# Kernel optimization log

Hardware: AMD Instinct MI355X
Metric: run time of the kernel (lower is better)

Reference implementation:

```python
import jax, jax.numpy as jnp
import numpy as np
import math

T, N, F, A, NH = 2048, 64, 64, 64, 8
QG, QH, DG, DH = 256, 256, 256, 256
HORIZON = 16


def setup_inputs() -> dict:
    key = jax.random.key(0)
    ks = jax.random.split(key, 12)
    s = 0.05  # xavier-ish scale
    return {
        "x_fix": jax.random.normal(ks[0], (T, F), jnp.float32),
        "x_att": jax.random.normal(ks[1], (T, N, A), jnp.float32),
        "train_horizon": HORIZON,
        # query GRUCell: input = fix + 2*A*NH
        "q_gru_w_ih": jax.random.normal(ks[2], (3 * QG, F + 2 * A * NH), jnp.float32) * s,
        "q_gru_w_hh": jax.random.normal(ks[3], (3 * QG, QG), jnp.float32) * s,
        "q_gru_b_ih": jnp.zeros((3 * QG,), jnp.float32),
        "q_gru_b_hh": jnp.zeros((3 * QG,), jnp.float32),
        # q_hidden: input = QG + F + A*NH
        "q_hid_w": jax.random.normal(ks[4], (QH, QG + F + A * NH), jnp.float32) * s,
        "q_hid_b": jnp.zeros((QH,), jnp.float32),
        "weight_q": jax.random.normal(ks[5], (QH, A * NH), jnp.float32) * s,
        # decoder GRU: input = F + A*NH
        "dec_gru_w_ih": jax.random.normal(ks[6], (3 * DG, F + A * NH), jnp.float32) * s,
        "dec_gru_w_hh": jax.random.normal(ks[7], (3 * DG, DG), jnp.float32) * s,
        "dec_gru_b_ih": jnp.zeros((3 * DG,), jnp.float32),
        "dec_gru_b_hh": jnp.zeros((3 * DG,), jnp.float32),
        # dec_hidden: input = DG + F + A*NH + A
        "dec_hid_w": jax.random.normal(ks[8], (DH, DG + F + A * NH + A), jnp.float32) * s,
        "dec_hid_b": jnp.zeros((DH,), jnp.float32),
        "dec_out_w": jax.random.normal(ks[9], (A, DH), jnp.float32) * s,
        "dec_out_b": jnp.zeros((A,), jnp.float32),
    }


def _gru_cell(x, h, w_ih, w_hh, b_ih, b_hh):
    """PyTorch GRUCell math (gate order r,z,n)."""
    gi = w_ih @ x + b_ih
    gh = w_hh @ h + b_hh
    ir, iz, in_ = jnp.split(gi, 3)
    hr, hz, hn = jnp.split(gh, 3)
    r = jax.nn.sigmoid(ir + hr)
    z = jax.nn.sigmoid(iz + hz)
    n = jnp.tanh(in_ + r * hn)
    return (1.0 - z) * n + z * h


def reference(x_fix, x_att, train_horizon,
              q_gru_w_ih, q_gru_w_hh, q_gru_b_ih, q_gru_b_hh,
              q_hid_w, q_hid_b, weight_q,
              dec_gru_w_ih, dec_gru_w_hh, dec_gru_b_ih, dec_gru_b_hh,
              dec_hid_w, dec_hid_b, dec_out_w, dec_out_b):
    t, n_obj, a = x_att.shape
    nh_a = weight_q.shape[1]
    nh = nh_a // a
    scale = 1.0 / math.sqrt(a)

    # ---- recurrent query generation (sequential over time) ----
    def step(carry, inp):
        h, query = carry
        fix_t, att_t = inp                                   # [F], [N, A]
        attw = jax.nn.softmax((query.reshape(nh, a) @ att_t.T) * scale, axis=1)  # [NH, N]
        att_v = (attw @ att_t).reshape(-1)                   # [NH*A]
        h2 = _gru_cell(jnp.concatenate([fix_t, att_v, query]), h,
                       q_gru_w_ih, q_gru_w_hh, q_gru_b_ih, q_gru_b_hh)
        hid = jax.nn.relu(q_hid_w @ jnp.concatenate([h2, fix_t, att_v]) + q_hid_b)
        query2 = hid @ weight_q
        return (h2, query2), (attw, att_v)

    h0 = jnp.zeros((q_gru_w_hh.shape[1],), x_fix.dtype)
    q0 = jnp.ones((nh_a,), x_fix.dtype)
    (q_gru_n, query_n), (attw, att_a) = jax.lax.scan(step, (h0, q0), (x_fix, x_att))

    # ---- decoder (training path; dropout_p=0, noise_std=0 -> identity) ----
    hz = train_horizon
    # replicate-pad attw back hz steps in time, drop last hz: dec_attw[t] = attw[max(t-hz,0)]
    dec_attw = jnp.concatenate(
        [jnp.broadcast_to(attw[:1], (hz,) + attw.shape[1:]), attw[:-hz]], axis=0)  # [T, NH, N]
    dec_att_a = jnp.einsum('thn,tnd->thd', dec_attw, x_att).reshape(t, -1)          # [T, NH*A]
    dec_x = jnp.concatenate([x_fix, dec_att_a], axis=-1)                            # [T, F+NH*A]

    def dec_step(hd, xt):
        hd2 = _gru_cell(xt, hd, dec_gru_w_ih, dec_gru_w_hh, dec_gru_b_ih, dec_gru_b_hh)
        return hd2, hd2

    dg0 = jnp.zeros((dec_gru_w_hh.shape[1],), x_fix.dtype)
    dec_gru_n, dec_gru_a = jax.lax.scan(dec_step, dg0, dec_x)                       # [T, DG]

    feat = jnp.concatenate([dec_gru_a, dec_x], axis=-1)                             # [T, DG+F+NH*A]
    feat_b = jnp.broadcast_to(feat[:, None, :], (t, n_obj, feat.shape[-1]))
    inp = jnp.concatenate([feat_b, x_att], axis=-1)                                 # [T, N, DG+F+NH*A+A]
    hid = jax.nn.relu(inp @ dec_hid_w.T + dec_hid_b)
    pred = jax.nn.relu(hid @ dec_out_w.T + dec_out_b)                               # [T, N, A]

    return pred, attw, q_gru_n, dec_gru_n, query_n
```

## Files before the change

kernel.cpp:

```cpp
#include <hip/hip_runtime.h>
#include <math.h>

#define TT 2048
#define HZ 16
#define NBLK 32
#define NTH 512

#define OUT_ATTW   (2048*64*64)
#define OUT_QGRU   (OUT_ATTW + 2048*8*64)
#define OUT_DECGRU (OUT_QGRU + 256)
#define OUT_QN     (OUT_DECGRU + 256)

#define WSO_MB1    0
#define WSO_QACC   8192
#define WSO_QCNT   14336
#define WSO_ZEND   14464
#define WSO_GIFIX  14464
#define WSO_HIDFIX (WSO_GIFIX + 2048*768*4)
#define WSO_W2T    (WSO_HIDFIX + 2048*256*4)
#define WSO_DAVA   (WSO_W2T + 256*64*4)
#define WSO_DECH   (WSO_DAVA + 2048*512*4)
#define WSO_FEAT   (WSO_DECH + 2048*256*4)
#define WSO_SBUF   (WSO_FEAT + 2048*832*4)

__device__ __forceinline__ float warp_sum(float v) {
#pragma unroll
  for (int o = 32; o > 0; o >>= 1) v += __shfl_down(v, o, 64);
  return v;
}
__device__ __forceinline__ float warp_max(float v) {
#pragma unroll
  for (int o = 32; o > 0; o >>= 1) v = fmaxf(v, __shfl_down(v, o, 64));
  return v;
}
__device__ __forceinline__ float sigf(float x) { return 1.f / (1.f + __expf(-x)); }
__device__ __forceinline__ float dot4(float4 a, float4 b) {
  return a.x*b.x + a.y*b.y + a.z*b.z + a.w*b.w;
}
__device__ __forceinline__ unsigned long long aload64(const unsigned long long* p) {
  return __hip_atomic_load(p, __ATOMIC_RELAXED, __HIP_MEMORY_SCOPE_AGENT);
}
__device__ __forceinline__ void astore64(unsigned long long* p, unsigned long long v) {
  __hip_atomic_store(p, v, __ATOMIC_RELAXED, __HIP_MEMORY_SCOPE_AGENT);
}
__device__ __forceinline__ unsigned long long mbpack(float f, unsigned tag) {
  return ((unsigned long long)tag << 32) | (unsigned long long)__float_as_uint(f);
}
__device__ __forceinline__ float mbpoll(const unsigned long long* p, unsigned tag) {
  unsigned long long v = aload64(p);
  while ((unsigned)(v >> 32) != tag) {
    __builtin_amdgcn_s_sleep(1);
    v = aload64(p);
  }
  return __uint_as_float((unsigned)v);
}

__global__ void transpose_k(const float* __restrict__ w2,
                            float* __restrict__ w2T) {
  int e = blockIdx.x * 256 + threadIdx.x;
  int r = e >> 6, a = e & 63;
  w2T[e] = w2[a * 256 + r];
}

__global__ void __launch_bounds__(256) gemm64(
    const float* __restrict__ X, int ldx,
    const float* __restrict__ W, int ldw, int woff,
    const float* __restrict__ bias,
    float* __restrict__ C, int crows, int K) {
  __shared__ float Xs[64 * 65];
  __shared__ float Ws[64 * 65];
  int t0 = blockIdx.x * 64, r0 = blockIdx.y * 64;
  int tid = threadIdx.x;
  int u = tid & 15, v = tid >> 4;
  float acc[4][4];
#pragma unroll
  for (int i = 0; i < 4; i++)
#pragma unroll
    for (int j = 0; j < 4; j++) acc[i][j] = 0.f;

  for (int kc = 0; kc < K; kc += 64) {
    for (int idx = tid; idx < 4096; idx += 256) {
      int row = idx >> 6, col = idx & 63;
      Xs[row * 65 + col] = X[(size_t)(t0 + row) * ldx + kc + col];
      Ws[row * 65 + col] = W[(size_t)(r0 + row) * ldw + woff + kc + col];
    }
    __syncthreads();
#pragma unroll 8
    for (int k = 0; k < 64; k++) {
      float xs[4], ws[4];
#pragma unroll
      for (int i = 0; i < 4; i++) xs[i] = Xs[(v + 16 * i) * 65 + k];
#pragma unroll
      for (int j = 0; j < 4; j++) ws[j] = Ws[(u + 16 * j) * 65 + k];
#pragma unroll
      for (int i = 0; i < 4; i++)
#pragma unroll
        for (int j = 0; j < 4; j++) acc[i][j] += xs[i] * ws[j];
    }
    __syncthreads();
  }
#pragma unroll
  for (int i = 0; i < 4; i++)
#pragma unroll
    for (int j = 0; j < 4; j++) {
      int t = t0 + v + 16 * i, r = r0 + u + 16 * j;
      C[(size_t)t * crows + r] = acc[i][j] + bias[r];
    }
}

__global__ void __launch_bounds__(512) seq_kernel(
    const float* __restrict__ x_fix,
    const float* __restrict__ x_att,
    const float* __restrict__ w_ih,
    const float* __restrict__ w_hh,
    const float* __restrict__ b_hh,
    const float* __restrict__ q_hid_w,
    const float* __restrict__ wq,
    const float* __restrict__ dwih,
    const float* __restrict__ dwhh,
    const float* __restrict__ dbih,
    const float* __restrict__ dbhh,
    const float* __restrict__ gi_fix,
    const float* __restrict__ hid_fix,
    unsigned long long* __restrict__ mb1,
    float* __restrict__ qacc,
    unsigned* __restrict__ qcnt,
    float* __restrict__ dava,
    float* __restrict__ dec_hist,
    float* __restrict__ out) {
  __shared__ float att_s[64 * 65];
  __shared__ float ring_s[16][512];
  __shared__ __align__(16) float avq_s[1024];
  __shared__ float qk_s[512];
  __shared__ __align__(16) float xcat_s[576];
  __shared__ __align__(16) float hid8_s[8];
  __shared__ __align__(16) float h_s[256];
  __shared__ __align__(16) float dech_s[256];
  __shared__ float g_s[4][8];
  __shared__ float dg_s[4][8];

  const int tid = threadIdx.x;
  const int bid = blockIdx.x;
  const int lane = tid & 63, wv = tid >> 6;

  int rowsQ[3];
#pragma unroll
  for (int k = 0; k < 3; k++) {
    int m = wv * 3 + k;
    rowsQ[k] = ((m >> 3) * 256) + bid * 8 + (m & 7);
  }

  float4 wGi[3][4];
  float4 wGh[3];
  float bhh_r[3], dbi_r[3], dbh_r[3];
#pragma unroll
  for (int k = 0; k < 3; k++) {
    const float4* Wi = (const float4*)(w_ih + (size_t)rowsQ[k] * 1088 + 64);
#pragma unroll
    for (int c0 = 0; c0 < 4; c0++) wGi[k][c0] = Wi[lane + 64 * c0];
    wGh[k] = ((const float4*)(w_hh + (size_t)rowsQ[k] * 256))[lane];
    bhh_r[k] = b_hh[rowsQ[k]];
    dbi_r[k] = dbih[rowsQ[k]];
    dbh_r[k] = dbhh[rowsQ[k]];
  }
  float4 wBq[3];
  {
    const float4* W = (const float4*)(q_hid_w + (size_t)(bid * 8 + wv) * 832);
    wBq[0] = W[lane];
    wBq[1] = W[80 + lane];
    wBq[2] = W[144 + lane];
  }
  float wqr[8];
#pragma unroll
  for (int r = 0; r < 8; r++) wqr[r] = wq[(size_t)(bid * 8 + r) * 512 + tid];

  auto dec_gates = [&]() {
    float accg[3], acch[3];
#pragma unroll
    for (int k = 0; k < 3; k++) { accg[k] = 0.f; acch[k] = 0.f; }
    const float4* x4 = (const float4*)xcat_s;
#pragma unroll
    for (int c0 = 0; c0 < 3; c0++) {
      int c = lane + 64 * c0;
      if (c < 144) {
        float4 v = x4[c];
#pragma unroll
        for (int k = 0; k < 3; k++) {
          const float4* W = (const float4*)(dwih + (size_t)rowsQ[k] * 576);
          accg[k] += dot4(W[c], v);
        }
      }
    }
    {
      float4 vh = ((const float4*)dech_s)[lane];
#pragma unroll
      for (int k = 0; k < 3; k++) {
        const float4* Wh = (const float4*)(dwhh + (size_t)rowsQ[k] * 256);
        acch[k] += dot4(Wh[lane], vh);
      }
    }
#pragma unroll
    for (int k = 0; k < 3; k++) {
      int m = wv * 3 + k;
      int gate = m >> 3, idx = m & 7;
      if (gate < 2) {
        float s = warp_sum(accg[k] + acch[k]);
        if (lane == 0) dg_s[gate][idx] = s + dbi_r[k] + dbh_r[k];
      } else {
        float sg = warp_sum(accg[k]);
        float sh = warp_sum(acch[k]);
        if (lane == 0) { dg_s[2][idx] = sg + dbi_r[k]; dg_s[3][idx] = sh + dbh_r[k]; }
      }
    }
  };

  for (int i = tid; i < 1024; i += NTH) avq_s[i] = (i >= 512) ? 1.f : 0.f;
  if (tid < 256) { h_s[tid] = 0.f; dech_s[tid] = 0.f; }
  {
    const float4* g4 = (const float4*)x_att;
    float4 a = g4[tid * 2], b = g4[tid * 2 + 1];
    int row = tid >> 3, c0 = (tid & 7) * 8;
    float* d = &att_s[row * 65 + c0];
    d[0]=a.x; d[1]=a.y; d[2]=a.z; d[3]=a.w; d[4]=b.x; d[5]=b.y; d[6]=b.z; d[7]=b.w;
  }
  if (tid < 64) xcat_s[tid] = x_fix[tid];
  __syncthreads();

  for (int t = 0; t <= TT; ++t) {
    if (t > 0) {
      {
        float f = mbpoll(mb1 + (size_t)((t - 1) & 1) * 512 + tid, (unsigned)t);
        int b = tid >> 4, j = tid & 15;
        if (j < 8) h_s[b * 8 + j] = f;
        else dech_s[b * 8 + j - 8] = f;
        if (t >= 2 && tid < 16)
          __hip_atomic_store(&qacc[(size_t)((t - 1) % 3) * 512 + bid * 16 + tid],
                             0.f, __ATOMIC_RELAXED, __HIP_MEMORY_SCOPE_AGENT);
      }
      __syncthreads();
      {
        float hfx = hid_fix[(size_t)(t - 1) * 256 + bid * 8 + wv];
        const float4* h4 = (const float4*)h_s;
        const float4* a4 = (const float4*)avq_s;
        float acc = dot4(wBq[0], h4[lane]) + dot4(wBq[1], a4[lane]) +
                    dot4(wBq[2], a4[64 + lane]);
        float s = warp_sum(acc);
        if (lane == 0) hid8_s[wv] = fmaxf(s + hfx, 0.f);
      }
      __syncthreads();
      {
        float hv[8];
#pragma unroll
        for (int r = 0; r < 8; r++) hv[r] = hid8_s[r];
        float partial = 0.f;
#pragma unroll
        for (int r = 0; r < 8; r++) partial += hv[r] * wqr[r];
        __hip_atomic_fetch_add(&qacc[(size_t)(t % 3) * 512 + tid], partial,
                               __ATOMIC_RELAXED, __HIP_MEMORY_SCOPE_AGENT);
        asm volatile("s_waitcnt vmcnt(0)" ::: "memory");
      }
      __syncthreads();
      if (tid == 0)
        __hip_atomic_fetch_add(qcnt, 1u, __ATOMIC_RELAXED,
                               __HIP_MEMORY_SCOPE_AGENT);
      if (t < TT) {
        {
          const float* rg = ring_s[(t >= 16) ? (t & 15) : 0];
          float dv = 0.f;
#pragma unroll 8
          for (int n = 0; n < 64; n++) dv += rg[wv * 64 + n] * att_s[n * 65 + lane];
          xcat_s[64 + wv * 64 + lane] = dv;
        }
        __syncthreads();
        dec_gates();
        __syncthreads();
        if (tid < 8) {
          float r = sigf(dg_s[0][tid]), z = sigf(dg_s[1][tid]);
          float nn = tanhf(dg_s[2][tid] + r * dg_s[3][tid]);
          float d2 = (1.f - z) * nn + z * dech_s[bid * 8 + tid];
          astore64(&mb1[(size_t)(t & 1) * 512 + bid * 16 + 8 + tid],
                   mbpack(d2, (unsigned)(t + 1)));
          dec_hist[(size_t)t * 256 + bid * 8 + tid] = d2;
        } else if (tid >= 16 && tid < 32) {
          int k2 = tid - 16;
          dava[(size_t)t * 512 + bid * 16 + k2] = xcat_s[64 + bid * 16 + k2];
        }
      }
      if (tid == 0) {
        unsigned target = 32u * (unsigned)t;
        while (__hip_atomic_load(qcnt, __ATOMIC_RELAXED,
                                 __HIP_MEMORY_SCOPE_AGENT) < target)
          __builtin_amdgcn_s_sleep(1);
      }
      __syncthreads();
      {
        float qv = __hip_atomic_load(&qacc[(size_t)(t % 3) * 512 + tid],
                                     __ATOMIC_RELAXED, __HIP_MEMORY_SCOPE_AGENT);
        avq_s[512 + tid] = qv;
        if (t == TT) {
          if (bid == 0) {
            if (tid < 256) {
              out[OUT_QGRU + tid] = h_s[tid];
              out[OUT_DECGRU + tid] = dech_s[tid];
            }
            out[OUT_QN + tid] = qv;
          }
          break;
        }
      }
      __syncthreads();
    }

    float4 pfa, pfb;
    {
      int tn = (t + 1 < TT) ? t + 1 : t;
      const float4* g4 = (const float4*)(x_att + (size_t)tn * 4096);
      pfa = g4[tid * 2];
      pfb = g4[tid * 2 + 1];
    }
    float gfx[3];
#pragma unroll
    for (int k = 0; k < 3; k++) gfx[k] = gi_fix[(size_t)t * 768 + rowsQ[k]];
    {
      float acc = 0.f;
#pragma unroll 16
      for (int a = 0; a < 64; a++)
        acc += avq_s[512 + wv * 64 + a] * att_s[lane * 65 + a];
      acc *= 0.125f;
      float m = __shfl(warp_max(acc), 0, 64);
      float e = __expf(acc - m);
      float s = __shfl(warp_sum(e), 0, 64);
      qk_s[wv * 64 + lane] = e / s;
    }
    {
      float av = 0.f;
#pragma unroll 8
      for (int n = 0; n < 64; n++)
        av += qk_s[wv * 64 + n] * att_s[n * 65 + lane];
      avq_s[wv * 64 + lane] = av;
    }
    if (t == 0) {
      float dv = 0.f;
#pragma unroll 8
      for (int n = 0; n < 64; n++)
        dv += qk_s[wv * 64 + n] * att_s[n * 65 + lane];
      xcat_s[64 + wv * 64 + lane] = dv;
    }
    __syncthreads();
    {
      float accg[3], acch[3];
#pragma unroll
      for (int k = 0; k < 3; k++) { accg[k] = 0.f; acch[k] = 0.f; }
      const float4* in4 = (const float4*)avq_s;
#pragma unroll
      for (int c0 = 0; c0 < 4; c0++) {
        float4 v = in4[lane + 64 * c0];
#pragma unroll
        for (int k = 0; k < 3; k++) accg[k] += dot4(wGi[k][c0], v);
      }
      {
        float4 vh = ((const float4*)h_s)[lane];
#pragma unroll
        for (int k = 0; k < 3; k++) acch[k] += dot4(wGh[k], vh);
      }
#pragma unroll
      for (int k = 0; k < 3; k++) {
        int m = wv * 3 + k;
        int gate = m >> 3, idx = m & 7;
        if (gate < 2) {
          float s = warp_sum(accg[k] + acch[k]);
          if (lane == 0) g_s[gate][idx] = s + gfx[k] + bhh_r[k];
        } else {
          float sg = warp_sum(accg[k]);
          float sh = warp_sum(acch[k]);
          if (lane == 0) { g_s[2][idx] = sg + gfx[k]; g_s[3][idx] = sh + bhh_r[k]; }
        }
      }
    }
    if (t == 0) dec_gates();
    __syncthreads();
    if (tid < 8) {
      float r = sigf(g_s[0][tid]), z = sigf(g_s[1][tid]);
      float nn = tanhf(g_s[2][tid] + r * g_s[3][tid]);
      float h2 = (1.f - z) * nn + z * h_s[bid * 8 + tid];
      astore64(&mb1[(size_t)(t & 1) * 512 + bid * 16 + tid],
               mbpack(h2, (unsigned)(t + 1)));
    } else if (t == 0 && tid < 16) {
      int i = tid - 8;
      float r = sigf(dg_s[0][i]), z = sigf(dg_s[1][i]);
      float nn = tanhf(dg_s[2][i] + r * dg_s[3][i]);
      float d2 = (1.f - z) * nn + z * dech_s[bid * 8 + i];
      astore64(&mb1[(size_t)(t & 1) * 512 + bid * 16 + tid],
               mbpack(d2, (unsigned)(t + 1)));
      dec_hist[(size_t)t * 256 + bid * 8 + i] = d2;
    }
    if (tid < 16) {
      out[OUT_ATTW + (size_t)t * 512 + bid * 16 + tid] = qk_s[bid * 16 + tid];
      if (t == 0)
        dava[(size_t)t * 512 + bid * 16 + tid] = xcat_s[64 + bid * 16 + tid];
    }
    ring_s[t & 15][tid] = qk_s[tid];
    {
      int row = tid >> 3, c0 = (tid & 7) * 8;
      float* d = &att_s[row * 65 + c0];
      d[0]=pfa.x; d[1]=pfa.y; d[2]=pfa.z; d[3]=pfa.w;
      d[4]=pfb.x; d[5]=pfb.y; d[6]=pfb.z; d[7]=pfb.w;
    }
    if (tid >= 448) {
      int i = tid - 448;
      int tn = (t + 1 < TT) ? t + 1 : t;
      xcat_s[i] = x_fix[tn * 64 + i];
    }
  }
}

__global__ void featcopy(const float* __restrict__ dec_hist,
                         const float* __restrict__ x_fix,
                         const float* __restrict__ dava,
                         float* __restrict__ feat) {
  int t = blockIdx.x, tid = threadIdx.x;
  float* f = feat + (size_t)t * 832;
  f[tid] = dec_hist[(size_t)t * 256 + tid];
  if (tid < 64) f[256 + tid] = x_fix[t * 64 + tid];
  for (int i = tid; i < 512; i += 256) f[320 + i] = dava[(size_t)t * 512 + i];
}

__global__ void __launch_bounds__(256) final_k(
    const float* __restrict__ x_att,
    const float* __restrict__ s,
    const float* __restrict__ w1,
    const float* __restrict__ w2T,
    const float* __restrict__ b2,
    float* __restrict__ pred) {
  __shared__ float att_s[4096];
  __shared__ float s_s[256];
  __shared__ float hid_s[32 * 256];
  int t = blockIdx.x, tid = threadIdx.x, lane = tid & 63, wv = tid >> 6;
  for (int i = tid; i < 4096; i += 256) att_s[i] = x_att[(size_t)t * 4096 + i];
  s_s[tid] = s[(size_t)t * 256 + tid];
  float4 w1v[16];
  const float4* W1a4 = (const float4*)(w1 + (size_t)tid * 896 + 832);
#pragma unroll
  for (int q = 0; q < 16; q++) w1v[q] = W1a4[q];
  float bb = b2[lane];
  __syncthreads();
  for (int ch = 0; ch < 2; ch++) {
    for (int nl = 0; nl < 32; nl++) {
      int n = ch * 32 + nl;
      const float4* a4 = (const float4*)(att_s + n * 64);
      float acc = s_s[tid];
#pragma unroll
      for (int q = 0; q < 16; q++) acc += dot4(w1v[q], a4[q]);
      hid_s[nl * 256 + tid] = fmaxf(acc, 0.f);
    }
    __syncthreads();
    float accb[8];
#pragma unroll
    for (int j = 0; j < 8; j++) accb[j] = bb;
    for (int r = 0; r < 256; r++) {
      float w = w2T[r * 64 + lane];
#pragma unroll
      for (int j = 0; j < 8; j++) accb[j] += w * hid_s[(wv * 8 + j) * 256 + r];
    }
#pragma unroll
    for (int j = 0; j < 8; j++) {
      int n = ch * 32 + wv * 8 + j;
      pred[(size_t)t * 4096 + n * 64 + lane] = fmaxf(accb[j], 0.f);
    }
    __syncthreads();
  }
}

extern "C" void kernel_launch(void* const* d_in, const int* in_sizes, int n_in,
                              void* d_out, int out_size, void* d_ws, size_t ws_size,
                              hipStream_t stream) {
  const float* x_fix = (const float*)d_in[0];
  const float* x_att = (const float*)d_in[1];
  const float* qwih = (const float*)d_in[3];
  const float* qwhh = (const float*)d_in[4];
  const float* qbih = (const float*)d_in[5];
  const float* qbhh = (const float*)d_in[6];
  const float* qhw = (const float*)d_in[7];
  const float* qhb = (const float*)d_in[8];
  const float* wq = (const float*)d_in[9];
  const float* dwih = (const float*)d_in[10];
  const float* dwhh = (const float*)d_in[11];
  const float* dbih = (const float*)d_in[12];
  const float* dbhh = (const float*)d_in[13];
  const float* w1 = (const float*)d_in[14];
  const float* b1 = (const float*)d_in[15];
  const float* w2 = (const float*)d_in[16];
  const float* b2 = (const float*)d_in[17];
  float* out = (float*)d_out;

  char* ws = (char*)d_ws;
  unsigned long long* mb1 = (unsigned long long*)(ws + WSO_MB1);
  float* qacc = (float*)(ws + WSO_QACC);
  unsigned* qcnt = (unsigned*)(ws + WSO_QCNT);
  float* gi_fix = (float*)(ws + WSO_GIFIX);
  float* hid_fix = (float*)(ws + WSO_HIDFIX);
  float* w2T = (float*)(ws + WSO_W2T);
  float* dava = (float*)(ws + WSO_DAVA);
  float* dec_hist = (float*)(ws + WSO_DECH);
  float* feat = (float*)(ws + WSO_FEAT);
  float* sbuf = (float*)(ws + WSO_SBUF);

  hipMemsetAsync(ws, 0, WSO_ZEND, stream);

  transpose_k<<<64, 256, 0, stream>>>(w2, w2T);
  gemm64<<<dim3(32, 12), 256, 0, stream>>>(x_fix, 64, qwih, 1088, 0, qbih,
                                           gi_fix, 768, 64);
  gemm64<<<dim3(32, 4), 256, 0, stream>>>(x_fix, 64, qhw, 832, 256, qhb,
                                          hid_fix, 256, 64);

  seq_kernel<<<NBLK, NTH, 0, stream>>>(x_fix, x_att, qwih, qwhh, qbhh,
                                       qhw, wq, dwih, dwhh, dbih, dbhh,
                                       gi_fix, hid_fix, mb1, qacc, qcnt,
                                       dava, dec_hist, out);

  featcopy<<<2048, 256, 0, stream>>>(dec_hist, x_fix, dava, feat);
  gemm64<<<dim3(32, 4), 256, 0, stream>>>(feat, 832, w1, 896, 0, b1,
                                          sbuf, 256, 832);
  final_k<<<2048, 256, 0, stream>>>(x_att, sbuf, w1, w2T, b2, out);
}
```

Baseline: 18.35 ms.

## Replace mailbox broadcast with atomic partial-sum accumulation and single barrier per step

The cross-block exchange in the sequential kernel is restructured. Each block no longer polls tagged mailboxes for the full hidden states. It scatters atomic partial products of its own 8 hidden units into triple-buffered global accumulators for the q_hidden input, the query GRU hh gates and the decoder GRU hh gates. Each timestep now needs only one grid-wide counter barrier instead of a mailbox poll plus a counter wait. The trade-off is many more global float atomics per step, and the final query product is now computed redundantly in every block from a transposed weight_q.

Measured after the change: 50.50 ms. 175% more time.

```diff
diff --git a/kernel.cpp b/kernel.cpp
--- a/kernel.cpp
+++ b/kernel.cpp
@@ -2,7 +2,6 @@
 #include <math.h>
 
 #define TT 2048
-#define HZ 16
 #define NBLK 32
 #define NTH 512
 
@@ -11,17 +10,19 @@
 #define OUT_DECGRU (OUT_QGRU + 256)
 #define OUT_QN     (OUT_DECGRU + 256)
 
-#define WSO_MB1    0
-#define WSO_QACC   8192
-#define WSO_QCNT   14336
-#define WSO_ZEND   14464
-#define WSO_GIFIX  14464
+#define WSO_QCNT   0
+#define WSO_HIDACC 128
+#define WSO_GHACC  3200
+#define WSO_DGHACC 12416
+#define WSO_ZEND   21632
+#define WSO_GIFIX  21632
 #define WSO_HIDFIX (WSO_GIFIX + 2048*768*4)
 #define WSO_W2T    (WSO_HIDFIX + 2048*256*4)
 #define WSO_DAVA   (WSO_W2T + 256*64*4)
 #define WSO_DECH   (WSO_DAVA + 2048*512*4)
 #define WSO_FEAT   (WSO_DECH + 2048*256*4)
 #define WSO_SBUF   (WSO_FEAT + 2048*832*4)
+#define WSO_WQT    WSO_FEAT
 
 __device__ __forceinline__ float warp_sum(float v) {
 #pragma unroll
@@ -37,22 +38,17 @@
 __device__ __forceinline__ float dot4(float4 a, float4 b) {
   return a.x*b.x + a.y*b.y + a.z*b.z + a.w*b.w;
 }
-__device__ __forceinline__ unsigned long long aload64(const unsigned long long* p) {
+__device__ __forceinline__ float aloadf(float* p) {
   return __hip_atomic_load(p, __ATOMIC_RELAXED, __HIP_MEMORY_SCOPE_AGENT);
 }
-__device__ __forceinline__ void astore64(unsigned long long* p, unsigned long long v) {
+__device__ __forceinline__ void astoref(float* p, float v) {
   __hip_atomic_store(p, v, __ATOMIC_RELAXED, __HIP_MEMORY_SCOPE_AGENT);
 }
-__device__ __forceinline__ unsigned long long mbpack(float f, unsigned tag) {
-  return ((unsigned long long)tag << 32) | (unsigned long long)__float_as_uint(f);
-}
-__device__ __forceinline__ float mbpoll(const unsigned long long* p, unsigned tag) {
-  unsigned long long v = aload64(p);
-  while ((unsigned)(v >> 32) != tag) {
-    __builtin_amdgcn_s_sleep(1);
-    v = aload64(p);
-  }
-  return __uint_as_float((unsigned)v);
+__device__ __forceinline__ void aaddf(float* p, float v) {
+  __hip_atomic_fetch_add(p, v, __ATOMIC_RELAXED, __HIP_MEMORY_SCOPE_AGENT);
+}
+__device__ __forceinline__ unsigned aloadu(unsigned* p) {
+  return __hip_atomic_load(p, __ATOMIC_RELAXED, __HIP_MEMORY_SCOPE_AGENT);
 }
 
 __global__ void transpose_k(const float* __restrict__ w2,
@@ -60,6 +56,12 @@
   int e = blockIdx.x * 256 + threadIdx.x;
   int r = e >> 6, a = e & 63;
   w2T[e] = w2[a * 256 + r];
+}
+
+__global__ void transpose_wq(const float* __restrict__ wq,
+                             float* __restrict__ wqT) {
+  wqT[(size_t)blockIdx.x * 256 + threadIdx.x] =
+      wq[(size_t)threadIdx.x * 512 + blockIdx.x];
 }
 
 __global__ void __launch_bounds__(256) gemm64(
@@ -115,15 +117,16 @@
     const float* __restrict__ w_hh,
     const float* __restrict__ b_hh,
     const float* __restrict__ q_hid_w,
-    const float* __restrict__ wq,
+    const float* __restrict__ wqT,
     const float* __restrict__ dwih,
     const float* __restrict__ dwhh,
     const float* __restrict__ dbih,
     const float* __restrict__ dbhh,
     const float* __restrict__ gi_fix,
     const float* __restrict__ hid_fix,
-    unsigned long long* __restrict__ mb1,
-    float* __restrict__ qacc,
+    float* __restrict__ hidacc,
+    float* __restrict__ ghacc,
+    float* __restrict__ dghacc,
     unsigned* __restrict__ qcnt,
     float* __restrict__ dava,
     float* __restrict__ dec_hist,
@@ -133,15 +136,16 @@
   __shared__ __align__(16) float avq_s[1024];
   __shared__ float qk_s[512];
   __shared__ __align__(16) float xcat_s[576];
-  __shared__ __align__(16) float hid8_s[8];
-  __shared__ __align__(16) float h_s[256];
-  __shared__ __align__(16) float dech_s[256];
+  __shared__ __align__(16) float hid_sh[256];
+  __shared__ float h_own_s[8];
+  __shared__ float dech_own_s[8];
   __shared__ float g_s[4][8];
   __shared__ float dg_s[4][8];
 
   const int tid = threadIdx.x;
   const int bid = blockIdx.x;
   const int lane = tid & 63, wv = tid >> 6;
+  const int r256 = tid & 255;
 
   int rowsQ[3];
 #pragma unroll
@@ -151,71 +155,41 @@
   }
 
   float4 wGi[3][4];
-  float4 wGh[3];
   float bhh_r[3], dbi_r[3], dbh_r[3];
 #pragma unroll
   for (int k = 0; k < 3; k++) {
     const float4* Wi = (const float4*)(w_ih + (size_t)rowsQ[k] * 1088 + 64);
 #pragma unroll
     for (int c0 = 0; c0 < 4; c0++) wGi[k][c0] = Wi[lane + 64 * c0];
-    wGh[k] = ((const float4*)(w_hh + (size_t)rowsQ[k] * 256))[lane];
     bhh_r[k] = b_hh[rowsQ[k]];
     dbi_r[k] = dbih[rowsQ[k]];
     dbh_r[k] = dbhh[rowsQ[k]];
   }
-  float4 wBq[3];
+  float4 wBq1, wBq2;
   {
     const float4* W = (const float4*)(q_hid_w + (size_t)(bid * 8 + wv) * 832);
-    wBq[0] = W[lane];
-    wBq[1] = W[80 + lane];
-    wBq[2] = W[144 + lane];
-  }
-  float wqr[8];
-#pragma unroll
-  for (int r = 0; r < 8; r++) wqr[r] = wq[(size_t)(bid * 8 + r) * 512 + tid];
-
-  auto dec_gates = [&]() {
-    float accg[3], acch[3];
-#pragma unroll
-    for (int k = 0; k < 3; k++) { accg[k] = 0.f; acch[k] = 0.f; }
-    const float4* x4 = (const float4*)xcat_s;
-#pragma unroll
-    for (int c0 = 0; c0 < 3; c0++) {
-      int c = lane + 64 * c0;
-      if (c < 144) {
-        float4 v = x4[c];
-#pragma unroll
-        for (int k = 0; k < 3; k++) {
-          const float4* W = (const float4*)(dwih + (size_t)rowsQ[k] * 576);
-          accg[k] += dot4(W[c], v);
-        }
-      }
-    }
-    {
-      float4 vh = ((const float4*)dech_s)[lane];
-#pragma unroll
-      for (int k = 0; k < 3; k++) {
-        const float4* Wh = (const float4*)(dwhh + (size_t)rowsQ[k] * 256);
-        acch[k] += dot4(Wh[lane], vh);
-      }
-    }
-#pragma unroll
-    for (int k = 0; k < 3; k++) {
-      int m = wv * 3 + k;
-      int gate = m >> 3, idx = m & 7;
-      if (gate < 2) {
-        float s = warp_sum(accg[k] + acch[k]);
-        if (lane == 0) dg_s[gate][idx] = s + dbi_r[k] + dbh_r[k];
-      } else {
-        float sg = warp_sum(accg[k]);
-        float sh = warp_sum(acch[k]);
-        if (lane == 0) { dg_s[2][idx] = sg + dbi_r[k]; dg_s[3][idx] = sh + dbh_r[k]; }
-      }
-    }
-  };
+    wBq1 = W[80 + lane];
+    wBq2 = W[144 + lane];
+  }
+  float qh8[8];
+  float whh1[8];
+  float whh2[8];
+  float dh1[8];
+  float dh2[8];
+#pragma unroll
+  for (int j = 0; j < 8; j++) {
+    qh8[j]  = q_hid_w[(size_t)r256 * 832 + bid * 8 + j];
+    whh1[j] = w_hh[(size_t)tid * 256 + bid * 8 + j];
+    whh2[j] = w_hh[(size_t)(512 + r256) * 256 + bid * 8 + j];
+    dh1[j]  = dwhh[(size_t)tid * 256 + bid * 8 + j];
+    dh2[j]  = dwhh[(size_t)(512 + r256) * 256 + bid * 8 + j];
+  }
+
+  float gh_r[3] = {0.f, 0.f, 0.f};
+  float dgh_r[3] = {0.f, 0.f, 0.f};
 
   for (int i = tid; i < 1024; i += NTH) avq_s[i] = (i >= 512) ? 1.f : 0.f;
-  if (tid < 256) { h_s[tid] = 0.f; dech_s[tid] = 0.f; }
+  if (tid < 8) { h_own_s[tid] = 0.f; dech_own_s[tid] = 0.f; }
   {
     const float4* g4 = (const float4*)x_att;
     float4 a = g4[tid * 2], b = g4[tid * 2 + 1];
@@ -228,85 +202,45 @@
 
   for (int t = 0; t <= TT; ++t) {
     if (t > 0) {
+      int p = t % 3, p0 = (t - 1) % 3;
       {
-        float f = mbpoll(mb1 + (size_t)((t - 1) & 1) * 512 + tid, (unsigned)t);
-        int b = tid >> 4, j = tid & 15;
-        if (j < 8) h_s[b * 8 + j] = f;
-        else dech_s[b * 8 + j - 8] = f;
-        if (t >= 2 && tid < 16)
-          __hip_atomic_store(&qacc[(size_t)((t - 1) % 3) * 512 + bid * 16 + tid],
-                             0.f, __ATOMIC_RELAXED, __HIP_MEMORY_SCOPE_AGENT);
-      }
+        unsigned target = 32u * (unsigned)t;
+        while (aloadu(qcnt) < target) __builtin_amdgcn_s_sleep(1);
+      }
+      float ha = 0.f;
+      if (tid < 256) ha = aloadf(hidacc + p * 256 + tid);
+      if (lane == 0) {
+#pragma unroll
+        for (int k = 0; k < 3; k++) {
+          gh_r[k]  = aloadf(ghacc  + p * 768 + rowsQ[k]);
+          dgh_r[k] = aloadf(dghacc + p * 768 + rowsQ[k]);
+        }
+      }
+      if (tid < 8) astoref(hidacc + p0 * 256 + bid * 8 + tid, 0.f);
+      if (lane == 0) {
+#pragma unroll
+        for (int k = 0; k < 3; k++) {
+          astoref(ghacc  + p0 * 768 + rowsQ[k], 0.f);
+          astoref(dghacc + p0 * 768 + rowsQ[k], 0.f);
+        }
+      }
+      if (tid < 256) hid_sh[tid] = fmaxf(ha, 0.f);
       __syncthreads();
+      float q = 0.f;
       {
-        float hfx = hid_fix[(size_t)(t - 1) * 256 + bid * 8 + wv];
-        const float4* h4 = (const float4*)h_s;
-        const float4* a4 = (const float4*)avq_s;
-        float acc = dot4(wBq[0], h4[lane]) + dot4(wBq[1], a4[lane]) +
-                    dot4(wBq[2], a4[64 + lane]);
-        float s = warp_sum(acc);
-        if (lane == 0) hid8_s[wv] = fmaxf(s + hfx, 0.f);
-      }
-      __syncthreads();
-      {
-        float hv[8];
-#pragma unroll
-        for (int r = 0; r < 8; r++) hv[r] = hid8_s[r];
-        float partial = 0.f;
-#pragma unroll
-        for (int r = 0; r < 8; r++) partial += hv[r] * wqr[r];
-        __hip_atomic_fetch_add(&qacc[(size_t)(t % 3) * 512 + tid], partial,
-                               __ATOMIC_RELAXED, __HIP_MEMORY_SCOPE_AGENT);
-        asm volatile("s_waitcnt vmcnt(0)" ::: "memory");
-      }
-      __syncthreads();
-      if (tid == 0)
-        __hip_atomic_fetch_add(qcnt, 1u, __ATOMIC_RELAXED,
-                               __HIP_MEMORY_SCOPE_AGENT);
-      if (t < TT) {
-        {
-          const float* rg = ring_s[(t >= 16) ? (t & 15) : 0];
-          float dv = 0.f;
+        const float4* wt = (const float4*)(wqT + (size_t)tid * 256);
+        const float4* h4 = (const float4*)hid_sh;
 #pragma unroll 8
-          for (int n = 0; n < 64; n++) dv += rg[wv * 64 + n] * att_s[n * 65 + lane];
-          xcat_s[64 + wv * 64 + lane] = dv;
+        for (int rr = 0; rr < 64; rr++) q += dot4(wt[rr], h4[rr]);
+      }
+      avq_s[512 + tid] = q;
+      if (t == TT) {
+        if (tid < 8) {
+          out[OUT_QGRU + bid * 8 + tid] = h_own_s[tid];
+          out[OUT_DECGRU + bid * 8 + tid] = dech_own_s[tid];
         }
-        __syncthreads();
-        dec_gates();
-        __syncthreads();
-        if (tid < 8) {
-          float r = sigf(dg_s[0][tid]), z = sigf(dg_s[1][tid]);
-          float nn = tanhf(dg_s[2][tid] + r * dg_s[3][tid]);
-          float d2 = (1.f - z) * nn + z * dech_s[bid * 8 + tid];
-          astore64(&mb1[(size_t)(t & 1) * 512 + bid * 16 + 8 + tid],
-                   mbpack(d2, (unsigned)(t + 1)));
-          dec_hist[(size_t)t * 256 + bid * 8 + tid] = d2;
-        } else if (tid >= 16 && tid < 32) {
-          int k2 = tid - 16;
-          dava[(size_t)t * 512 + bid * 16 + k2] = xcat_s[64 + bid * 16 + k2];
-        }
-      }
-      if (tid == 0) {
-        unsigned target = 32u * (unsigned)t;
-        while (__hip_atomic_load(qcnt, __ATOMIC_RELAXED,
-                                 __HIP_MEMORY_SCOPE_AGENT) < target)
-          __builtin_amdgcn_s_sleep(1);
-      }
-      __syncthreads();
-      {
-        float qv = __hip_atomic_load(&qacc[(size_t)(t % 3) * 512 + tid],
-                                     __ATOMIC_RELAXED, __HIP_MEMORY_SCOPE_AGENT);
-        avq_s[512 + tid] = qv;
-        if (t == TT) {
-          if (bid == 0) {
-            if (tid < 256) {
-              out[OUT_QGRU + tid] = h_s[tid];
-              out[OUT_DECGRU + tid] = dech_s[tid];
-            }
-            out[OUT_QN + tid] = qv;
-          }
-          break;
-        }
+        if (bid == 0) out[OUT_QN + tid] = q;
+        break;
       }
       __syncthreads();
     }
@@ -339,65 +273,134 @@
         av += qk_s[wv * 64 + n] * att_s[n * 65 + lane];
       avq_s[wv * 64 + lane] = av;
     }
-    if (t == 0) {
-      float dv = 0.f;
-#pragma unroll 8
-      for (int n = 0; n < 64; n++)
-        dv += qk_s[wv * 64 + n] * att_s[n * 65 + lane];
-      xcat_s[64 + wv * 64 + lane] = dv;
-    }
-    __syncthreads();
-    {
-      float accg[3], acch[3];
-#pragma unroll
-      for (int k = 0; k < 3; k++) { accg[k] = 0.f; acch[k] = 0.f; }
+    __syncthreads();
+    {
+      float accg[3];
+#pragma unroll
+      for (int k = 0; k < 3; k++) accg[k] = 0.f;
       const float4* in4 = (const float4*)avq_s;
 #pragma unroll
       for (int c0 = 0; c0 < 4; c0++) {
         float4 v = in4[lane + 64 * c0];
 #pragma unroll
         for (int k = 0; k < 3; k++) accg[k] += dot4(wGi[k][c0], v);
-      }
-      {
-        float4 vh = ((const float4*)h_s)[lane];
-#pragma unroll
-        for (int k = 0; k < 3; k++) acch[k] += dot4(wGh[k], vh);
       }
 #pragma unroll
       for (int k = 0; k < 3; k++) {
         int m = wv * 3 + k;
         int gate = m >> 3, idx = m & 7;
         if (gate < 2) {
-          float s = warp_sum(accg[k] + acch[k]);
-          if (lane == 0) g_s[gate][idx] = s + gfx[k] + bhh_r[k];
+          float s = warp_sum(accg[k]);
+          if (lane == 0) g_s[gate][idx] = s + gh_r[k] + gfx[k] + bhh_r[k];
         } else {
           float sg = warp_sum(accg[k]);
-          float sh = warp_sum(acch[k]);
-          if (lane == 0) { g_s[2][idx] = sg + gfx[k]; g_s[3][idx] = sh + bhh_r[k]; }
+          if (lane == 0) {
+            g_s[2][idx] = sg + gfx[k];
+            g_s[3][idx] = gh_r[k] + bhh_r[k];
+          }
         }
       }
     }
-    if (t == 0) dec_gates();
     __syncthreads();
     if (tid < 8) {
       float r = sigf(g_s[0][tid]), z = sigf(g_s[1][tid]);
       float nn = tanhf(g_s[2][tid] + r * g_s[3][tid]);
-      float h2 = (1.f - z) * nn + z * h_s[bid * 8 + tid];
-      astore64(&mb1[(size_t)(t & 1) * 512 + bid * 16 + tid],
-               mbpack(h2, (unsigned)(t + 1)));
-    } else if (t == 0 && tid < 16) {
-      int i = tid - 8;
-      float r = sigf(dg_s[0][i]), z = sigf(dg_s[1][i]);
-      float nn = tanhf(dg_s[2][i] + r * dg_s[3][i]);
-      float d2 = (1.f - z) * nn + z * dech_s[bid * 8 + i];
-      astore64(&mb1[(size_t)(t & 1) * 512 + bid * 16 + tid],
-               mbpack(d2, (unsigned)(t + 1)));
-      dec_hist[(size_t)t * 256 + bid * 8 + i] = d2;
-    }
-    if (tid < 16) {
+      h_own_s[tid] = (1.f - z) * nn + z * h_own_s[tid];
+    }
+    __syncthreads();
+    int pn = (t + 1) % 3;
+    if (tid < 256) {
+      float part = 0.f;
+#pragma unroll
+      for (int j = 0; j < 8; j++) part += qh8[j] * h_own_s[j];
+      aaddf(hidacc + pn * 256 + tid, part);
+    }
+    {
+      const float4* a4 = (const float4*)avq_s;
+      float acc = dot4(wBq1, a4[lane]) + dot4(wBq2, a4[64 + lane]);
+      float s = warp_sum(acc);
+      if (lane == 0)
+        aaddf(hidacc + pn * 256 + bid * 8 + wv,
+              s + hid_fix[(size_t)t * 256 + bid * 8 + wv]);
+    }
+    {
+      float p1 = 0.f;
+#pragma unroll
+      for (int j = 0; j < 8; j++) p1 += whh1[j] * h_own_s[j];
+      aaddf(ghacc + pn * 768 + tid, p1);
+      if (tid < 256) {
+        float p2 = 0.f;
+#pragma unroll
+        for (int j = 0; j < 8; j++) p2 += whh2[j] * h_own_s[j];
+        aaddf(ghacc + pn * 768 + 512 + tid, p2);
+      }
+    }
+    {
+      const float* rg = (t == 0) ? &qk_s[0] : ring_s[(t >= 16) ? (t & 15) : 0];
+      float dv = 0.f;
+#pragma unroll 8
+      for (int n = 0; n < 64; n++) dv += rg[wv * 64 + n] * att_s[n * 65 + lane];
+      xcat_s[64 + wv * 64 + lane] = dv;
+    }
+    __syncthreads();
+    {
+      float accg[3];
+#pragma unroll
+      for (int k = 0; k < 3; k++) accg[k] = 0.f;
+      const float4* x4 = (const float4*)xcat_s;
+#pragma unroll
+      for (int c0 = 0; c0 < 3; c0++) {
+        int c = lane + 64 * c0;
+        if (c < 144) {
+          float4 v = x4[c];
+#pragma unroll
+          for (int k = 0; k < 3; k++) {
+            const float4* W = (const float4*)(dwih + (size_t)rowsQ[k] * 576);
+            accg[k] += dot4(W[c], v);
+          }
+        }
+      }
+#pragma unroll
+      for (int k = 0; k < 3; k++) {
+        int m = wv * 3 + k;
+        int gate = m >> 3, idx = m & 7;
+        if (gate < 2) {
+          float s = warp_sum(accg[k]);
+          if (lane == 0) dg_s[gate][idx] = s + dgh_r[k] + dbi_r[k] + dbh_r[k];
+        } else {
+          float sg = warp_sum(accg[k]);
+          if (lane == 0) {
+            dg_s[2][idx] = sg + dbi_r[k];
+            dg_s[3][idx] = dgh_r[k] + dbh_r[k];
+          }
+        }
+      }
+    }
+    __syncthreads();
+    if (tid < 8) {
+      float r = sigf(dg_s[0][tid]), z = sigf(dg_s[1][tid]);
+      float nn = tanhf(dg_s[2][tid] + r * dg_s[3][tid]);
+      float d2 = (1.f - z) * nn + z * dech_own_s[tid];
+      dech_own_s[tid] = d2;
+      dec_hist[(size_t)t * 256 + bid * 8 + tid] = d2;
+    } else if (tid >= 16 && tid < 32) {
+      int k2 = tid - 16;
+      dava[(size_t)t * 512 + bid * 16 + k2] = xcat_s[64 + bid * 16 + k2];
+    }
+    if (tid < 16)
       out[OUT_ATTW + (size_t)t * 512 + bid * 16 + tid] = qk_s[bid * 16 + tid];
-      if (t == 0)
-        dava[(size_t)t * 512 + bid * 16 + tid] = xcat_s[64 + bid * 16 + tid];
+    __syncthreads();
+    {
+      float p1 = 0.f;
+#pragma unroll
+      for (int j = 0; j < 8; j++) p1 += dh1[j] * dech_own_s[j];
+      aaddf(dghacc + pn * 768 + tid, p1);
+      if (tid < 256) {
+        float p2 = 0.f;
+#pragma unroll
+        for (int j = 0; j < 8; j++) p2 += dh2[j] * dech_own_s[j];
+        aaddf(dghacc + pn * 768 + 512 + tid, p2);
+      }
     }
     ring_s[t & 15][tid] = qk_s[tid];
     {
@@ -411,6 +414,11 @@
       int tn = (t + 1 < TT) ? t + 1 : t;
       xcat_s[i] = x_fix[tn * 64 + i];
     }
+    asm volatile("s_waitcnt vmcnt(0)" ::: "memory");
+    __syncthreads();
+    if (tid == 0)
+      __hip_atomic_fetch_add(qcnt, 1u, __ATOMIC_RELAXED,
+                             __HIP_MEMORY_SCOPE_AGENT);
   }
 }
 
@@ -494,9 +502,10 @@
   float* out = (float*)d_out;
 
   char* ws = (char*)d_ws;
-  unsigned long long* mb1 = (unsigned long long*)(ws + WSO_MB1);
-  float* qacc = (float*)(ws + WSO_QACC);
   unsigned* qcnt = (unsigned*)(ws + WSO_QCNT);
+  float* hidacc = (float*)(ws + WSO_HIDACC);
+  float* ghacc = (float*)(ws + WSO_GHACC);
+  float* dghacc = (float*)(ws + WSO_DGHACC);
   float* gi_fix = (float*)(ws + WSO_GIFIX);
   float* hid_fix = (float*)(ws + WSO_HIDFIX);
   float* w2T = (float*)(ws + WSO_W2T);
@@ -504,19 +513,21 @@
   float* dec_hist = (float*)(ws + WSO_DECH);
   float* feat = (float*)(ws + WSO_FEAT);
   float* sbuf = (float*)(ws + WSO_SBUF);
+  float* wqT = (float*)(ws + WSO_WQT);
 
   hipMemsetAsync(ws, 0, WSO_ZEND, stream);
 
   transpose_k<<<64, 256, 0, stream>>>(w2, w2T);
+  transpose_wq<<<512, 256, 0, stream>>>(wq, wqT);
   gemm64<<<dim3(32, 12), 256, 0, stream>>>(x_fix, 64, qwih, 1088, 0, qbih,
                                            gi_fix, 768, 64);
   gemm64<<<dim3(32, 4), 256, 0, stream>>>(x_fix, 64, qhw, 832, 256, qhb,
                                           hid_fix, 256, 64);
 
   seq_kernel<<<NBLK, NTH, 0, stream>>>(x_fix, x_att, qwih, qwhh, qbhh,
-                                       qhw, wq, dwih, dwhh, dbih, dbhh,
-                                       gi_fix, hid_fix, mb1, qacc, qcnt,
-                                       dava, dec_hist, out);
+                                       qhw, wqT, dwih, dwhh, dbih, dbhh,
+                                       gi_fix, hid_fix, hidacc, ghacc, dghacc,
+                                       qcnt, dava, dec_hist, out);
 
   featcopy<<<2048, 256, 0, stream>>>(dec_hist, x_fix, dava, feat);
   gemm64<<<dim3(32, 4), 256, 0, stream>>>(feat, 832, w1, 896, 0, b1,
```
